# Kernel optimization log

Hardware: AMD Instinct MI355X
Metric: run time of the kernel (lower is better)

Reference implementation:

```python
import jax, jax.numpy as jnp
import numpy as np

DIM = 1024
NUM_HEADS = 16
SEQ_LEN = 4096


def setup_inputs() -> dict:
    key = jax.random.key(0)
    ks = jax.random.split(key, 9)
    s = DIM ** -0.5  # typical init scale for weights
    return {
        "x": jax.random.normal(ks[0], (SEQ_LEN, DIM), dtype=jnp.float32),
        "Wq": jax.random.normal(ks[1], (DIM, DIM), dtype=jnp.float32) * s,
        "bq": jax.random.normal(ks[2], (DIM,), dtype=jnp.float32) * s,
        "Wk": jax.random.normal(ks[3], (DIM, DIM), dtype=jnp.float32) * s,
        "bk": jax.random.normal(ks[4], (DIM,), dtype=jnp.float32) * s,
        "Wv": jax.random.normal(ks[5], (DIM, DIM), dtype=jnp.float32) * s,
        "bv": jax.random.normal(ks[6], (DIM,), dtype=jnp.float32) * s,
        "Wp": jax.random.normal(ks[7], (DIM, DIM), dtype=jnp.float32) * s,
        "bp": jax.random.normal(ks[8], (DIM,), dtype=jnp.float32) * s,
    }


def reference(x, Wq, bq, Wk, bk, Wv, bv, Wp, bp):
    T, C = x.shape
    H = NUM_HEADS
    Dh = C // H
    # QKV projections (eqx.nn.Linear: y = W @ x + b, vmapped over tokens)
    q = (x @ Wq.T + bq).reshape(T, H, Dh).swapaxes(0, 1)  # [H, T, Dh]
    k = (x @ Wk.T + bk).reshape(T, H, Dh).swapaxes(0, 1)
    v = (x @ Wv.T + bv).reshape(T, H, Dh).swapaxes(0, 1)
    # NOTE: original scales by C**-0.5 (full dim), not head_dim**-0.5
    attn = jnp.einsum("htd,hsd->hts", q, k) * (C ** -0.5)  # [H, T, T]
    causal = jnp.tril(jnp.ones((T, T), dtype=bool))[None, :, :]
    attn = jnp.where(causal, attn, -jnp.inf)
    attn = jax.nn.softmax(attn, axis=-1)
    out = jnp.einsum("hts,hsd->htd", attn, v)  # [H, T, Dh]
    out = out.swapaxes(0, 1).reshape(T, C)
    return out @ Wp.T + bp
```

## Files before the change

kernel.cpp:

```cpp
#include <hip/hip_runtime.h>
#include <stdint.h>

typedef unsigned short u16;
typedef __bf16 bf16x8 __attribute__((ext_vector_type(8)));
typedef u16 u16x8 __attribute__((ext_vector_type(8)));
typedef u16 u16x4 __attribute__((ext_vector_type(4)));
typedef float f32x4 __attribute__((ext_vector_type(4)));
typedef float f32x16 __attribute__((ext_vector_type(16)));

#define SEQ 4096
#define CD 1024
#define NH 16
#define DHD 64

__device__ __forceinline__ u16 f2bf(float f) {
  union { float f; unsigned u; } v; v.f = f;
  unsigned r = v.u + 0x7fffu + ((v.u >> 16) & 1u);
  return (u16)(r >> 16);
}
__device__ __forceinline__ unsigned fbits(float f) {
  union { float f; unsigned u; } v; v.f = f; return v.u;
}
__device__ __forceinline__ float fexp2(float x) {
#if __has_builtin(__builtin_amdgcn_exp2f)
  return __builtin_amdgcn_exp2f(x);
#else
  return exp2f(x);
#endif
}

__device__ __forceinline__ void load_lds16(const u16* g, u16* l) {
  __builtin_amdgcn_global_load_lds((const __attribute__((address_space(1))) void*)g,
                                   (__attribute__((address_space(3))) void*)l, 16, 0, 0);
}

__global__ __launch_bounds__(256) void cvt_all(const float* __restrict__ x, const float* __restrict__ Wq,
                                               const float* __restrict__ Wk, const float* __restrict__ Wv,
                                               const float* __restrict__ Wp,
                                               u16* __restrict__ xb, u16* __restrict__ Wb, u16* __restrict__ Wpb) {
  int b = blockIdx.x;
  const float* src; u16* dst; int base;
  if (b < 2048)      { src = x;  dst = xb;             base = b; }
  else if (b < 2560) { src = Wq; dst = Wb;             base = b - 2048; }
  else if (b < 3072) { src = Wk; dst = Wb + CD * CD;   base = b - 2560; }
  else if (b < 3584) { src = Wv; dst = Wb + 2*CD*CD;   base = b - 3072; }
  else               { src = Wp; dst = Wpb;            base = b - 3584; }
  int i = (base * 256 + (int)threadIdx.x) * 8;
  float4 a = *(const float4*)(src + i);
  float4 c = *(const float4*)(src + i + 4);
  u16x8 o;
  o[0] = f2bf(a.x); o[1] = f2bf(a.y); o[2] = f2bf(a.z); o[3] = f2bf(a.w);
  o[4] = f2bf(c.x); o[5] = f2bf(c.y); o[6] = f2bf(c.z); o[7] = f2bf(c.w);
  *(u16x8*)(dst + i) = o;
}

template<int MODE>
__device__ __forceinline__ void gemm_core(const u16* __restrict__ A, const u16* __restrict__ Bw,
                                          const float* __restrict__ bias, void* __restrict__ outp,
                                          float oscale) {
  constexpr int K = CD, N = CD;
  __shared__ u16 As[128 * 32];
  __shared__ u16 Bs[128 * 32];
  const int tid = threadIdx.x;
  const int w = tid >> 6, L = tid & 63, q = L >> 4, ln = L & 15;
  const int rowA0 = blockIdx.y * 128, rowB0 = blockIdx.x * 128;
  const int wr = (w >> 1) * 64, wc = (w & 1) * 64;
  f32x4 acc[4][4] = {};
  for (int k0 = 0; k0 < K; k0 += 32) {
#pragma unroll
    for (int pass = 0; pass < 2; ++pass) {
      int off = pass * 4096 + tid * 16;
      int row = off >> 6;
      int cole = (off & 63) >> 1;
      load_lds16(A + (size_t)(rowA0 + row) * K + k0 + cole, As + pass * 2048 + w * 512);
      load_lds16(Bw + (size_t)(rowB0 + row) * K + k0 + cole, Bs + pass * 2048 + w * 512);
    }
    __syncthreads();
    bf16x8 af[4], bg[4];
#pragma unroll
    for (int i = 0; i < 4; ++i) af[i] = *(const bf16x8*)(As + (wr + i * 16 + ln) * 32 + q * 8);
#pragma unroll
    for (int i = 0; i < 4; ++i) bg[i] = *(const bf16x8*)(Bs + (wc + i * 16 + ln) * 32 + q * 8);
#pragma unroll
    for (int i = 0; i < 4; ++i)
#pragma unroll
      for (int j = 0; j < 4; ++j)
        acc[i][j] = __builtin_amdgcn_mfma_f32_16x16x32_bf16(af[i], bg[j], acc[i][j], 0, 0, 0);
    __syncthreads();
  }
#pragma unroll
  for (int i = 0; i < 4; ++i) {
#pragma unroll
    for (int j = 0; j < 4; ++j) {
      int col = rowB0 + wc + j * 16 + ln;
      float bb = bias[col];
#pragma unroll
      for (int r = 0; r < 4; ++r) {
        int row = rowA0 + wr + i * 16 + q * 4 + r;
        float v = (acc[i][j][r] + bb) * oscale;
        if (MODE == 0)      ((u16*)outp)[(size_t)row * N + col] = f2bf(v);
        else if (MODE == 1) ((u16*)outp)[(size_t)col * SEQ + row] = f2bf(v);
        else                ((float*)outp)[(size_t)row * N + col] = v;
      }
    }
  }
}

__global__ __launch_bounds__(256) void gemm_qkv(const u16* __restrict__ A, const u16* __restrict__ W3,
                                                const float* __restrict__ bq, const float* __restrict__ bk,
                                                const float* __restrict__ bv, u16* __restrict__ Qb,
                                                u16* __restrict__ Kb, u16* __restrict__ VTb) {
  int z = blockIdx.z;
  if (z == 0)      gemm_core<0>(A, W3,               bq, Qb,  0.0450842200f);
  else if (z == 1) gemm_core<0>(A, W3 + CD * CD,     bk, Kb,  1.0f);
  else             gemm_core<1>(A, W3 + 2 * CD * CD, bv, VTb, 1.0f);
}

__global__ __launch_bounds__(256) void gemm_proj(const u16* __restrict__ A, const u16* __restrict__ Bw,
                                                 const float* __restrict__ bias, float* __restrict__ out) {
  gemm_core<2>(A, Bw, bias, out, 1.0f);
}

__global__ __launch_bounds__(256, 3) void attn_kernel(const u16* __restrict__ Q, const u16* __restrict__ Kg,
                                                      const u16* __restrict__ VTg, u16* __restrict__ O) {
  __shared__ u16 Ks[2][64 * 72];
  __shared__ u16 Vt[2][64 * 72];
  const int tid = threadIdx.x, w = tid >> 6, L = tid & 63;
  const int ln = L & 31, hh = L >> 5;
  const int p = w >> 1, sub = w & 1;
  const int b = blockIdx.x;
  const int qt = (SEQ / 64 - 1) - (b >> 4);
  const int h = b & 15;
  const int colH = h * DHD;
  const int qrow0 = qt * 64 + sub * 32;
  const int nt0 = (qt + 2) >> 1;
  int jt = p ? nt0 : 0;
  const int jt_end = p ? (qt + 1) : nt0;
  bf16x8 qf[4];
#pragma unroll
  for (int kk = 0; kk < 4; ++kk)
    qf[kk] = *(const bf16x8*)(Q + (size_t)(qrow0 + ln) * CD + colH + kk * 16 + hh * 8);
  f32x16 oa[2] = {};
  f32x4 lsv = {};
  const int ptid = tid & 127;
  const int srow = ptid >> 3, sx = ptid & 7;
  u16* KsP = Ks[p];
  u16* VtP = Vt[p];
  u16x8 kr[4], vr[4];
  bool active = jt < jt_end;
  if (active) {
#pragma unroll
    for (int c = 0; c < 4; ++c) {
      kr[c] = *(const u16x8*)(Kg + (size_t)(jt * 64 + c * 16 + srow) * CD + colH + sx * 8);
      vr[c] = *(const u16x8*)(VTg + (size_t)(colH + c * 16 + srow) * SEQ + jt * 64 + sx * 8);
    }
  }
  for (int i = 0; i < nt0; ++i) {
    if (active) {
#pragma unroll
      for (int c = 0; c < 4; ++c) {
        *(u16x8*)(KsP + (c * 16 + srow) * 72 + sx * 8) = kr[c];
        *(u16x8*)(VtP + (c * 16 + srow) * 72 + sx * 8) = vr[c];
      }
    }
    __syncthreads();
    const bool hasnext = (jt + 1) < jt_end;
    if (hasnext) {
      const size_t kb2 = (size_t)(jt + 1) * 64;
#pragma unroll
      for (int c = 0; c < 4; ++c) {
        kr[c] = *(const u16x8*)(Kg + (kb2 + c * 16 + srow) * CD + colH + sx * 8);
        vr[c] = *(const u16x8*)(VTg + (size_t)(colH + c * 16 + srow) * SEQ + kb2 + sx * 8);
      }
    }
    if (active) {
      const bool diag = (jt == qt);
#pragma unroll
      for (int nt = 0; nt < 2; ++nt) {
        f32x16 a = {};
        __builtin_amdgcn_s_setprio(1);
#pragma unroll
        for (int kk = 0; kk < 4; ++kk) {
          bf16x8 kf = *(const bf16x8*)(KsP + (nt * 32 + ln) * 72 + kk * 16 + hh * 8);
          a = __builtin_amdgcn_mfma_f32_32x32x16_bf16(kf, qf[kk], a, 0, 0, 0);
        }
        __builtin_amdgcn_s_setprio(0);
#pragma unroll
        for (int r = 0; r < 16; ++r) {
          float sv = a[r];
          if (diag) {
            const int key_l = nt * 32 + (r & 3) + 8 * (r >> 2) + 4 * hh;
            if (key_l > sub * 32 + ln) sv = -1e30f;
          }
          float pe = fexp2(sv);
          lsv[r & 3] += pe;
          a[r] = pe;
        }
        unsigned pk[8];
#pragma unroll
        for (int i2 = 0; i2 < 8; ++i2)
          pk[i2] = __builtin_amdgcn_perm(fbits(a[2 * i2 + 1]), fbits(a[2 * i2]), 0x07060302);
#pragma unroll
        for (int b0 = 0; b0 < 8; b0 += 4) {
          asm("v_permlane32_swap_b32 %0, %1" : "+v"(pk[b0 + 0]), "+v"(pk[b0 + 2]));
          asm("v_permlane32_swap_b32 %0, %1" : "+v"(pk[b0 + 1]), "+v"(pk[b0 + 3]));
        }
        __builtin_amdgcn_s_setprio(1);
#pragma unroll
        for (int g = 0; g < 2; ++g)
#pragma unroll
          for (int s2 = 0; s2 < 2; ++s2) {
            const int s = nt * 2 + s2;
            bf16x8 vf = *(const bf16x8*)(VtP + (g * 32 + ln) * 72 + s * 16 + hh * 8);
            union { unsigned u[4]; bf16x8 v; } pf;
            pf.u[0] = pk[s2 * 4 + 0]; pf.u[1] = pk[s2 * 4 + 1];
            pf.u[2] = pk[s2 * 4 + 2]; pf.u[3] = pk[s2 * 4 + 3];
            oa[g] = __builtin_amdgcn_mfma_f32_32x32x16_bf16(vf, pf.v, oa[g], 0, 0, 0);
          }
        __builtin_amdgcn_s_setprio(0);
      }
    }
    __syncthreads();
    ++jt;
    active = active && (jt < jt_end);
  }
  float lsum = (lsv[0] + lsv[1]) + (lsv[2] + lsv[3]);
  float* red = (float*)Ks;
  if (p == 1) {
    float* dst = red + ptid * 33;
#pragma unroll
    for (int g = 0; g < 2; ++g)
#pragma unroll
      for (int r = 0; r < 16; ++r) dst[g * 16 + r] = oa[g][r];
    dst[32] = lsum;
  }
  __syncthreads();
  if (p == 0) {
    const float* src = red + ptid * 33;
#pragma unroll
    for (int g = 0; g < 2; ++g)
#pragma unroll
      for (int r = 0; r < 16; ++r) oa[g][r] += src[g * 16 + r];
    lsum += src[32];
    lsum += __shfl_xor(lsum, 32, 64);
    const float inv = 1.0f / lsum;
#pragma unroll
    for (int g = 0; g < 2; ++g)
#pragma unroll
      for (int rg = 0; rg < 4; ++rg) {
        u16x4 ov;
#pragma unroll
        for (int i2 = 0; i2 < 4; ++i2) ov[i2] = f2bf(oa[g][rg * 4 + i2] * inv);
        *(u16x4*)(O + (size_t)(qrow0 + ln) * CD + colH + g * 32 + 8 * rg + 4 * hh) = ov;
      }
  }
}

extern "C" void kernel_launch(void* const* d_in, const int* in_sizes, int n_in,
                              void* d_out, int out_size, void* d_ws, size_t ws_size,
                              hipStream_t stream) {
  const float* x  = (const float*)d_in[0];
  const float* Wq = (const float*)d_in[1];
  const float* bq = (const float*)d_in[2];
  const float* Wk = (const float*)d_in[3];
  const float* bk = (const float*)d_in[4];
  const float* Wv = (const float*)d_in[5];
  const float* bv = (const float*)d_in[6];
  const float* Wp = (const float*)d_in[7];
  const float* bp = (const float*)d_in[8];

  char* ws = (char*)d_ws;
  u16* xb  = (u16*)(ws);
  u16* Wb  = (u16*)(ws + (8u << 20));
  u16* Wpb = (u16*)(ws + (14u << 20));
  u16* Qb  = (u16*)(ws + (16u << 20));
  u16* Kb  = (u16*)(ws + (24u << 20));
  u16* VTb = (u16*)(ws + (32u << 20));
  u16* Ab  = (u16*)(ws + (40u << 20));

  cvt_all<<<4096, 256, 0, stream>>>(x, Wq, Wk, Wv, Wp, xb, Wb, Wpb);
  gemm_qkv<<<dim3(CD / 128, SEQ / 128, 3), 256, 0, stream>>>(xb, Wb, bq, bk, bv, Qb, Kb, VTb);
  attn_kernel<<<(SEQ / 64) * NH, 256, 0, stream>>>(Qb, Kb, VTb, Ab);
  gemm_proj<<<dim3(CD / 128, SEQ / 128), 256, 0, stream>>>(Ab, Wpb, bp, (float*)d_out);
}
```

Baseline: 204.0 us.

## Template GEMM tiles, widen K-step to 64, add LDS XOR swizzle, vectorize V^T stores

Templates the shared GEMM core on output-tile width and K-step. The K-step doubles to 64, and LDS rows get an XOR swizzle to avoid bank conflicts on the fragment reads. The projection GEMM switches to 128x64 tiles to launch more blocks. The transposed V output now uses 4-wide vector stores. This costs more LDS per block and adds per-variant template code.

```diff
diff --git a/kernel.cpp b/kernel.cpp
--- a/kernel.cpp
+++ b/kernel.cpp
@@ -54,53 +54,75 @@
   *(u16x8*)(dst + i) = o;
 }
 
-template<int MODE>
-__device__ __forceinline__ void gemm_core(const u16* __restrict__ A, const u16* __restrict__ Bw,
+template<int MODE, int BN, int BKv>
+__device__ __forceinline__ void gemm_core(u16* As, u16* Bs,
+                                          const u16* __restrict__ A, const u16* __restrict__ Bw,
                                           const float* __restrict__ bias, void* __restrict__ outp,
                                           float oscale) {
   constexpr int K = CD, N = CD;
-  __shared__ u16 As[128 * 32];
-  __shared__ u16 Bs[128 * 32];
+  constexpr int ROWB = 2 * BKv;
+  constexpr int PA = (128 * ROWB) / 4096;
+  constexpr int PB = (BN * ROWB) / 4096;
+  constexpr int NJ = BN / 32;
+  constexpr int SWM = (ROWB >= 128) ? 7 : (ROWB / 16 - 1);
   const int tid = threadIdx.x;
   const int w = tid >> 6, L = tid & 63, q = L >> 4, ln = L & 15;
-  const int rowA0 = blockIdx.y * 128, rowB0 = blockIdx.x * 128;
-  const int wr = (w >> 1) * 64, wc = (w & 1) * 64;
-  f32x4 acc[4][4] = {};
-  for (int k0 = 0; k0 < K; k0 += 32) {
-#pragma unroll
-    for (int pass = 0; pass < 2; ++pass) {
+  const int rowA0 = blockIdx.y * 128, rowB0 = blockIdx.x * BN;
+  const int wr = (w >> 1) * 64, wc = (w & 1) * (BN / 2);
+  const int sw = (ln & SWM) << 4;
+  f32x4 acc[4][NJ] = {};
+  for (int k0 = 0; k0 < K; k0 += BKv) {
+#pragma unroll
+    for (int pass = 0; pass < PA; ++pass) {
       int off = pass * 4096 + tid * 16;
-      int row = off >> 6;
-      int cole = (off & 63) >> 1;
-      load_lds16(A + (size_t)(rowA0 + row) * K + k0 + cole, As + pass * 2048 + w * 512);
-      load_lds16(Bw + (size_t)(rowB0 + row) * K + k0 + cole, Bs + pass * 2048 + w * 512);
+      int row = off / ROWB;
+      int cb = (off & (ROWB - 1)) ^ ((row & SWM) << 4);
+      load_lds16(A + (size_t)(rowA0 + row) * K + k0 + (cb >> 1), As + pass * 2048 + w * 512);
+    }
+#pragma unroll
+    for (int pass = 0; pass < PB; ++pass) {
+      int off = pass * 4096 + tid * 16;
+      int row = off / ROWB;
+      int cb = (off & (ROWB - 1)) ^ ((row & SWM) << 4);
+      load_lds16(Bw + (size_t)(rowB0 + row) * K + k0 + (cb >> 1), Bs + pass * 2048 + w * 512);
     }
     __syncthreads();
-    bf16x8 af[4], bg[4];
-#pragma unroll
-    for (int i = 0; i < 4; ++i) af[i] = *(const bf16x8*)(As + (wr + i * 16 + ln) * 32 + q * 8);
-#pragma unroll
-    for (int i = 0; i < 4; ++i) bg[i] = *(const bf16x8*)(Bs + (wc + i * 16 + ln) * 32 + q * 8);
-#pragma unroll
-    for (int i = 0; i < 4; ++i)
-#pragma unroll
-      for (int j = 0; j < 4; ++j)
-        acc[i][j] = __builtin_amdgcn_mfma_f32_16x16x32_bf16(af[i], bg[j], acc[i][j], 0, 0, 0);
+#pragma unroll
+    for (int kk = 0; kk < BKv / 32; ++kk) {
+      bf16x8 af[4], bg[NJ];
+#pragma unroll
+      for (int i = 0; i < 4; ++i)
+        af[i] = *(const bf16x8*)((const char*)As + (size_t)(wr + i * 16 + ln) * ROWB + ((kk * 64 + q * 16) ^ sw));
+#pragma unroll
+      for (int j = 0; j < NJ; ++j)
+        bg[j] = *(const bf16x8*)((const char*)Bs + (size_t)(wc + j * 16 + ln) * ROWB + ((kk * 64 + q * 16) ^ sw));
+#pragma unroll
+      for (int i = 0; i < 4; ++i)
+#pragma unroll
+        for (int j = 0; j < NJ; ++j)
+          acc[i][j] = __builtin_amdgcn_mfma_f32_16x16x32_bf16(af[i], bg[j], acc[i][j], 0, 0, 0);
+    }
     __syncthreads();
   }
 #pragma unroll
   for (int i = 0; i < 4; ++i) {
 #pragma unroll
-    for (int j = 0; j < 4; ++j) {
+    for (int j = 0; j < NJ; ++j) {
       int col = rowB0 + wc + j * 16 + ln;
       float bb = bias[col];
-#pragma unroll
-      for (int r = 0; r < 4; ++r) {
-        int row = rowA0 + wr + i * 16 + q * 4 + r;
-        float v = (acc[i][j][r] + bb) * oscale;
-        if (MODE == 0)      ((u16*)outp)[(size_t)row * N + col] = f2bf(v);
-        else if (MODE == 1) ((u16*)outp)[(size_t)col * SEQ + row] = f2bf(v);
-        else                ((float*)outp)[(size_t)row * N + col] = v;
+      if (MODE == 1) {
+        u16x4 ov;
+#pragma unroll
+        for (int r = 0; r < 4; ++r) ov[r] = f2bf((acc[i][j][r] + bb) * oscale);
+        *(u16x4*)((u16*)outp + (size_t)col * SEQ + rowA0 + wr + i * 16 + q * 4) = ov;
+      } else {
+#pragma unroll
+        for (int r = 0; r < 4; ++r) {
+          int row = rowA0 + wr + i * 16 + q * 4 + r;
+          float v = (acc[i][j][r] + bb) * oscale;
+          if (MODE == 0) ((u16*)outp)[(size_t)row * N + col] = f2bf(v);
+          else           ((float*)outp)[(size_t)row * N + col] = v;
+        }
       }
     }
   }
@@ -110,15 +132,19 @@
                                                 const float* __restrict__ bq, const float* __restrict__ bk,
                                                 const float* __restrict__ bv, u16* __restrict__ Qb,
                                                 u16* __restrict__ Kb, u16* __restrict__ VTb) {
+  __shared__ __align__(16) u16 As[128 * 64];
+  __shared__ __align__(16) u16 Bs[128 * 64];
   int z = blockIdx.z;
-  if (z == 0)      gemm_core<0>(A, W3,               bq, Qb,  0.0450842200f);
-  else if (z == 1) gemm_core<0>(A, W3 + CD * CD,     bk, Kb,  1.0f);
-  else             gemm_core<1>(A, W3 + 2 * CD * CD, bv, VTb, 1.0f);
+  if (z == 0)      gemm_core<0, 128, 64>(As, Bs, A, W3,              bq, Qb,  0.0450842200f);
+  else if (z == 1) gemm_core<0, 128, 64>(As, Bs, A, W3 + CD * CD,    bk, Kb,  1.0f);
+  else             gemm_core<1, 128, 64>(As, Bs, A, W3 + 2 * CD * CD, bv, VTb, 1.0f);
 }
 
 __global__ __launch_bounds__(256) void gemm_proj(const u16* __restrict__ A, const u16* __restrict__ Bw,
                                                  const float* __restrict__ bias, float* __restrict__ out) {
-  gemm_core<2>(A, Bw, bias, out, 1.0f);
+  __shared__ __align__(16) u16 As[128 * 64];
+  __shared__ __align__(16) u16 Bs[64 * 64];
+  gemm_core<2, 64, 64>(As, Bs, A, Bw, bias, out, 1.0f);
 }
 
 __global__ __launch_bounds__(256, 3) void attn_kernel(const u16* __restrict__ Q, const u16* __restrict__ Kg,
@@ -281,5 +307,5 @@
   cvt_all<<<4096, 256, 0, stream>>>(x, Wq, Wk, Wv, Wp, xb, Wb, Wpb);
   gemm_qkv<<<dim3(CD / 128, SEQ / 128, 3), 256, 0, stream>>>(xb, Wb, bq, bk, bv, Qb, Kb, VTb);
   attn_kernel<<<(SEQ / 64) * NH, 256, 0, stream>>>(Qb, Kb, VTb, Ab);
-  gemm_proj<<<dim3(CD / 128, SEQ / 128), 256, 0, stream>>>(Ab, Wpb, bp, (float*)d_out);
-}
+  gemm_proj<<<dim3(CD / 64, SEQ / 128), 256, 0, stream>>>(Ab, Wpb, bp, (float*)d_out);
+}
```

Result: slower. 213.3 us (+4.6%).

## Double-buffer K tiles in LDS and load V fragments directly from global

Applied to the files above, without the earlier changes.

Attention K tiles now use two LDS buffers per pipeline half, prefetched two tiles ahead, so each iteration needs one barrier instead of two. V^T fragments are no longer staged through shared memory: each wave loads its MFMA operands straight from global memory. The causal-mask branch is hoisted out of the exp loop. This trades LDS traffic and a barrier for uncoalesced, uncached-in-LDS global reads of V, which each wave in the block fetches redundantly and which add latency right before the PV MFMAs.

```diff
diff --git a/kernel.cpp b/kernel.cpp
--- a/kernel.cpp
+++ b/kernel.cpp
@@ -123,8 +123,7 @@
 
 __global__ __launch_bounds__(256, 3) void attn_kernel(const u16* __restrict__ Q, const u16* __restrict__ Kg,
                                                       const u16* __restrict__ VTg, u16* __restrict__ O) {
-  __shared__ u16 Ks[2][64 * 72];
-  __shared__ u16 Vt[2][64 * 72];
+  __shared__ u16 Ks[2][2][64 * 72];
   const int tid = threadIdx.x, w = tid >> 6, L = tid & 63;
   const int ln = L & 31, hh = L >> 5;
   const int p = w >> 1, sub = w & 1;
@@ -134,8 +133,8 @@
   const int colH = h * DHD;
   const int qrow0 = qt * 64 + sub * 32;
   const int nt0 = (qt + 2) >> 1;
-  int jt = p ? nt0 : 0;
-  const int jt_end = p ? (qt + 1) : nt0;
+  const int jt0 = p ? nt0 : 0;
+  const int jte = p ? (qt + 1) : nt0;
   bf16x8 qf[4];
 #pragma unroll
   for (int kk = 0; kk < 4; ++kk)
@@ -144,36 +143,35 @@
   f32x4 lsv = {};
   const int ptid = tid & 127;
   const int srow = ptid >> 3, sx = ptid & 7;
-  u16* KsP = Ks[p];
-  u16* VtP = Vt[p];
-  u16x8 kr[4], vr[4];
-  bool active = jt < jt_end;
-  if (active) {
-#pragma unroll
-    for (int c = 0; c < 4; ++c) {
-      kr[c] = *(const u16x8*)(Kg + (size_t)(jt * 64 + c * 16 + srow) * CD + colH + sx * 8);
-      vr[c] = *(const u16x8*)(VTg + (size_t)(colH + c * 16 + srow) * SEQ + jt * 64 + sx * 8);
-    }
+  u16x8 kr[4];
+  if (jt0 < jte) {
+#pragma unroll
+    for (int c = 0; c < 4; ++c)
+      kr[c] = *(const u16x8*)(Kg + (size_t)(jt0 * 64 + c * 16 + srow) * CD + colH + sx * 8);
+#pragma unroll
+    for (int c = 0; c < 4; ++c)
+      *(u16x8*)(Ks[p][0] + (c * 16 + srow) * 72 + sx * 8) = kr[c];
+  }
+  if (jt0 + 1 < jte) {
+#pragma unroll
+    for (int c = 0; c < 4; ++c)
+      kr[c] = *(const u16x8*)(Kg + (size_t)((jt0 + 1) * 64 + c * 16 + srow) * CD + colH + sx * 8);
   }
   for (int i = 0; i < nt0; ++i) {
-    if (active) {
-#pragma unroll
-      for (int c = 0; c < 4; ++c) {
-        *(u16x8*)(KsP + (c * 16 + srow) * 72 + sx * 8) = kr[c];
-        *(u16x8*)(VtP + (c * 16 + srow) * 72 + sx * 8) = vr[c];
-      }
-    }
     __syncthreads();
-    const bool hasnext = (jt + 1) < jt_end;
-    if (hasnext) {
-      const size_t kb2 = (size_t)(jt + 1) * 64;
-#pragma unroll
-      for (int c = 0; c < 4; ++c) {
-        kr[c] = *(const u16x8*)(Kg + (kb2 + c * 16 + srow) * CD + colH + sx * 8);
-        vr[c] = *(const u16x8*)(VTg + (size_t)(colH + c * 16 + srow) * SEQ + kb2 + sx * 8);
-      }
-    }
-    if (active) {
+    const int jt = jt0 + i;
+    if (jt + 1 < jte) {
+#pragma unroll
+      for (int c = 0; c < 4; ++c)
+        *(u16x8*)(Ks[p][(i + 1) & 1] + (c * 16 + srow) * 72 + sx * 8) = kr[c];
+    }
+    if (jt + 2 < jte) {
+#pragma unroll
+      for (int c = 0; c < 4; ++c)
+        kr[c] = *(const u16x8*)(Kg + (size_t)((jt + 2) * 64 + c * 16 + srow) * CD + colH + sx * 8);
+    }
+    if (jt < jte) {
+      const u16* KsC = Ks[p][i & 1];
       const bool diag = (jt == qt);
 #pragma unroll
       for (int nt = 0; nt < 2; ++nt) {
@@ -181,20 +179,33 @@
         __builtin_amdgcn_s_setprio(1);
 #pragma unroll
         for (int kk = 0; kk < 4; ++kk) {
-          bf16x8 kf = *(const bf16x8*)(KsP + (nt * 32 + ln) * 72 + kk * 16 + hh * 8);
+          bf16x8 kf = *(const bf16x8*)(KsC + (nt * 32 + ln) * 72 + kk * 16 + hh * 8);
           a = __builtin_amdgcn_mfma_f32_32x32x16_bf16(kf, qf[kk], a, 0, 0, 0);
         }
         __builtin_amdgcn_s_setprio(0);
-#pragma unroll
-        for (int r = 0; r < 16; ++r) {
-          float sv = a[r];
-          if (diag) {
-            const int key_l = nt * 32 + (r & 3) + 8 * (r >> 2) + 4 * hh;
-            if (key_l > sub * 32 + ln) sv = -1e30f;
+        bf16x8 vfa[2][2];
+#pragma unroll
+        for (int g = 0; g < 2; ++g)
+#pragma unroll
+          for (int s2 = 0; s2 < 2; ++s2)
+            vfa[g][s2] = *(const bf16x8*)(VTg + (size_t)(colH + g * 32 + ln) * SEQ +
+                                          jt * 64 + (nt * 2 + s2) * 16 + hh * 8);
+        if (diag) {
+          const int thr = sub * 32 + ln - 4 * hh - nt * 32;
+#pragma unroll
+          for (int r = 0; r < 16; ++r) {
+            const int kl = (r & 3) + 8 * (r >> 2);
+            float pe = fexp2(kl > thr ? -1e30f : a[r]);
+            lsv[r & 3] += pe;
+            a[r] = pe;
           }
-          float pe = fexp2(sv);
-          lsv[r & 3] += pe;
-          a[r] = pe;
+        } else {
+#pragma unroll
+          for (int r = 0; r < 16; ++r) {
+            float pe = fexp2(a[r]);
+            lsv[r & 3] += pe;
+            a[r] = pe;
+          }
         }
         unsigned pk[8];
 #pragma unroll
@@ -210,20 +221,16 @@
         for (int g = 0; g < 2; ++g)
 #pragma unroll
           for (int s2 = 0; s2 < 2; ++s2) {
-            const int s = nt * 2 + s2;
-            bf16x8 vf = *(const bf16x8*)(VtP + (g * 32 + ln) * 72 + s * 16 + hh * 8);
             union { unsigned u[4]; bf16x8 v; } pf;
             pf.u[0] = pk[s2 * 4 + 0]; pf.u[1] = pk[s2 * 4 + 1];
             pf.u[2] = pk[s2 * 4 + 2]; pf.u[3] = pk[s2 * 4 + 3];
-            oa[g] = __builtin_amdgcn_mfma_f32_32x32x16_bf16(vf, pf.v, oa[g], 0, 0, 0);
+            oa[g] = __builtin_amdgcn_mfma_f32_32x32x16_bf16(vfa[g][s2], pf.v, oa[g], 0, 0, 0);
           }
         __builtin_amdgcn_s_setprio(0);
       }
     }
-    __syncthreads();
-    ++jt;
-    active = active && (jt < jt_end);
-  }
+  }
+  __syncthreads();
   float lsum = (lsv[0] + lsv[1]) + (lsv[2] + lsv[3]);
   float* red = (float*)Ks;
   if (p == 1) {
```

New measurement: 225.9 us. +10.7%, slower.

## Double-buffer LDS tiles in GEMM core to overlap loads with MFMA

Applied to the files above, without the earlier changes.

The shared-memory A/B tiles in the projection GEMMs are double-buffered. Each iteration prefetches the next K-slice into the alternate buffer while MFMAs run on the current one, so one barrier per iteration replaces two. The goal is to hide global-to-LDS latency behind compute. The cost is twice the LDS per block, which may lower occupancy, and the prefetched loads depend on the barrier waiting for outstanding async LDS loads.

```diff
diff --git a/kernel.cpp b/kernel.cpp
--- a/kernel.cpp
+++ b/kernel.cpp
@@ -55,38 +55,46 @@
 }
 
 template<int MODE>
-__device__ __forceinline__ void gemm_core(const u16* __restrict__ A, const u16* __restrict__ Bw,
+__device__ __forceinline__ void gemm_core(u16* As, u16* Bs,
+                                          const u16* __restrict__ A, const u16* __restrict__ Bw,
                                           const float* __restrict__ bias, void* __restrict__ outp,
                                           float oscale) {
   constexpr int K = CD, N = CD;
-  __shared__ u16 As[128 * 32];
-  __shared__ u16 Bs[128 * 32];
+  constexpr int NT = K / 32;
   const int tid = threadIdx.x;
   const int w = tid >> 6, L = tid & 63, q = L >> 4, ln = L & 15;
   const int rowA0 = blockIdx.y * 128, rowB0 = blockIdx.x * 128;
   const int wr = (w >> 1) * 64, wc = (w & 1) * 64;
+  const int soff0 = tid * 16, soff1 = 4096 + tid * 16;
+  const int srow0 = soff0 >> 6, scol0 = (soff0 & 63) >> 1;
+  const int srow1 = soff1 >> 6, scol1 = (soff1 & 63) >> 1;
+  const int sdst = w * 512;
   f32x4 acc[4][4] = {};
-  for (int k0 = 0; k0 < K; k0 += 32) {
-#pragma unroll
-    for (int pass = 0; pass < 2; ++pass) {
-      int off = pass * 4096 + tid * 16;
-      int row = off >> 6;
-      int cole = (off & 63) >> 1;
-      load_lds16(A + (size_t)(rowA0 + row) * K + k0 + cole, As + pass * 2048 + w * 512);
-      load_lds16(Bw + (size_t)(rowB0 + row) * K + k0 + cole, Bs + pass * 2048 + w * 512);
-    }
+  load_lds16(A + (size_t)(rowA0 + srow0) * K + scol0, As + sdst);
+  load_lds16(Bw + (size_t)(rowB0 + srow0) * K + scol0, Bs + sdst);
+  load_lds16(A + (size_t)(rowA0 + srow1) * K + scol1, As + 2048 + sdst);
+  load_lds16(Bw + (size_t)(rowB0 + srow1) * K + scol1, Bs + 2048 + sdst);
+  for (int it = 0; it < NT; ++it) {
     __syncthreads();
+    const int cur = (it & 1) * 4096;
+    if (it + 1 < NT) {
+      const int k0n = (it + 1) * 32;
+      const int nxt = cur ^ 4096;
+      load_lds16(A + (size_t)(rowA0 + srow0) * K + k0n + scol0, As + nxt + sdst);
+      load_lds16(Bw + (size_t)(rowB0 + srow0) * K + k0n + scol0, Bs + nxt + sdst);
+      load_lds16(A + (size_t)(rowA0 + srow1) * K + k0n + scol1, As + nxt + 2048 + sdst);
+      load_lds16(Bw + (size_t)(rowB0 + srow1) * K + k0n + scol1, Bs + nxt + 2048 + sdst);
+    }
     bf16x8 af[4], bg[4];
 #pragma unroll
-    for (int i = 0; i < 4; ++i) af[i] = *(const bf16x8*)(As + (wr + i * 16 + ln) * 32 + q * 8);
-#pragma unroll
-    for (int i = 0; i < 4; ++i) bg[i] = *(const bf16x8*)(Bs + (wc + i * 16 + ln) * 32 + q * 8);
+    for (int i = 0; i < 4; ++i) af[i] = *(const bf16x8*)(As + cur + (wr + i * 16 + ln) * 32 + q * 8);
+#pragma unroll
+    for (int i = 0; i < 4; ++i) bg[i] = *(const bf16x8*)(Bs + cur + (wc + i * 16 + ln) * 32 + q * 8);
 #pragma unroll
     for (int i = 0; i < 4; ++i)
 #pragma unroll
       for (int j = 0; j < 4; ++j)
         acc[i][j] = __builtin_amdgcn_mfma_f32_16x16x32_bf16(af[i], bg[j], acc[i][j], 0, 0, 0);
-    __syncthreads();
   }
 #pragma unroll
   for (int i = 0; i < 4; ++i) {
@@ -110,15 +118,19 @@
                                                 const float* __restrict__ bq, const float* __restrict__ bk,
                                                 const float* __restrict__ bv, u16* __restrict__ Qb,
                                                 u16* __restrict__ Kb, u16* __restrict__ VTb) {
+  __shared__ __align__(16) u16 As[2 * 128 * 32];
+  __shared__ __align__(16) u16 Bs[2 * 128 * 32];
   int z = blockIdx.z;
-  if (z == 0)      gemm_core<0>(A, W3,               bq, Qb,  0.0450842200f);
-  else if (z == 1) gemm_core<0>(A, W3 + CD * CD,     bk, Kb,  1.0f);
-  else             gemm_core<1>(A, W3 + 2 * CD * CD, bv, VTb, 1.0f);
+  if (z == 0)      gemm_core<0>(As, Bs, A, W3,               bq, Qb,  0.0450842200f);
+  else if (z == 1) gemm_core<0>(As, Bs, A, W3 + CD * CD,     bk, Kb,  1.0f);
+  else             gemm_core<1>(As, Bs, A, W3 + 2 * CD * CD, bv, VTb, 1.0f);
 }
 
 __global__ __launch_bounds__(256) void gemm_proj(const u16* __restrict__ A, const u16* __restrict__ Bw,
                                                  const float* __restrict__ bias, float* __restrict__ out) {
-  gemm_core<2>(A, Bw, bias, out, 1.0f);
+  __shared__ __align__(16) u16 As[2 * 128 * 32];
+  __shared__ __align__(16) u16 Bs[2 * 128 * 32];
+  gemm_core<2>(As, Bs, A, Bw, bias, out, 1.0f);
 }
 
 __global__ __launch_bounds__(256, 3) void attn_kernel(const u16* __restrict__ Q, const u16* __restrict__ Kg,
```

Result: slower. 214.2 us (+5.0%).
